# Optimization experiments

Measured on AMD Instinct MI355X. Metric: run time of the kernel, lower is better.

Reference implementation:

```python
import jax, jax.numpy as jnp
import numpy as np

B, S, D, H, E, K, F = 8, 2048, 1024, 16, 32, 8, 1024
HD = D // H
EPS = 1e-5


def _ln(x, scale, bias):
    m = jnp.mean(x, axis=-1, keepdims=True)
    v = jnp.mean(jnp.square(x - m), axis=-1, keepdims=True)
    return (x - m) * jax.lax.rsqrt(v + EPS) * scale + bias


def setup_inputs() -> dict:
    key = jax.random.key(0)
    ks = jax.random.split(key, 14)
    w = lambda k, shp: jax.random.normal(k, shp, jnp.float32) * 0.02
    return {
        "hidden_states": jax.random.normal(ks[0], (B, S, D), jnp.float32),
        "ln1_scale": jnp.ones((D,), jnp.float32),
        "ln1_bias": jnp.zeros((D,), jnp.float32),
        "wq": w(ks[1], (D, D)), "bq": jnp.zeros((D,), jnp.float32),
        "wk": w(ks[2], (D, D)), "bk": jnp.zeros((D,), jnp.float32),
        "wv": w(ks[3], (D, D)), "bv": jnp.zeros((D,), jnp.float32),
        "ln2_scale": jnp.ones((D,), jnp.float32),
        "ln2_bias": jnp.zeros((D,), jnp.float32),
        "router_w": w(ks[4], (D, E)), "router_b": jnp.zeros((E,), jnp.float32),
        "w1": w(ks[5], (E, D, F)), "b1": jnp.zeros((E, F), jnp.float32),
        "w2": w(ks[6], (E, F, D)), "b2": jnp.zeros((E, D), jnp.float32),
    }


def reference(hidden_states, ln1_scale, ln1_bias, wq, bq, wk, bk, wv, bv,
              ln2_scale, ln2_bias, router_w, router_b, w1, b1, w2, b2):
    # --- attention sub-block (faithful to source: scores are [B,S,H,H]) ---
    x = _ln(hidden_states, ln1_scale, ln1_bias)
    q = (x @ wq + bq).reshape(B, S, H, HD)
    k = (x @ wk + bk).reshape(B, S, H, HD)
    v = (x @ wv + bv).reshape(B, S, H, HD)
    scores = jnp.einsum('bshd,bsgd->bshg', q, k) / np.sqrt(HD).astype(np.float32)
    probs = jax.nn.softmax(scores, axis=-1)
    ctx = jnp.einsum('bshg,bsgd->bshd', probs, v).reshape(B, S, D)
    h1 = hidden_states + ctx
    # --- MoE sub-block: per-token top-K of E experts ---
    x2 = _ln(h1, ln2_scale, ln2_bias)
    router_probs = jax.nn.softmax(x2 @ router_w + router_b, axis=-1)  # [B,S,E]
    top_w, top_i = jax.lax.top_k(router_probs, K)
    top_w = top_w / jnp.sum(top_w, axis=-1, keepdims=True)
    # dense per-token gate over experts (zero for unselected)
    gates = jnp.sum(jax.nn.one_hot(top_i, E, dtype=x2.dtype) * top_w[..., None], axis=-2)  # [B,S,E]
    moe = jnp.zeros_like(x2)
    for e in range(E):  # fixed small expert set; unrolled under jit
        h = jax.nn.gelu(x2 @ w1[e] + b1[e], approximate=False)
        moe = moe + gates[..., e:e + 1] * (h @ w2[e] + b2[e])
    return h1 + moe
```

## Files before the change

### kernel.cpp

```cpp
#include <hip/hip_runtime.h>
#include <hip/hip_bf16.h>
#include <stdint.h>

#define TOK 16384
#define DD  1024
#define NE  32

typedef unsigned short u16;
typedef __attribute__((ext_vector_type(8))) short short8;
typedef __attribute__((ext_vector_type(4))) float f32x4;

__device__ __forceinline__ u16 f2bf(float f) {
  unsigned int u = __float_as_uint(f);
  u += 0x7fffu + ((u >> 16) & 1u);
  return (u16)(u >> 16);
}
__device__ __forceinline__ float bf2f(u16 h) {
  return __uint_as_float(((unsigned int)h) << 16);
}
__device__ __forceinline__ void gload16(const void* g, void* l) {
  __builtin_amdgcn_global_load_lds((const __attribute__((address_space(1))) void*)g,
                                   (__attribute__((address_space(3))) void*)l, 16, 0, 0);
}
__device__ __forceinline__ float fast_gelu(float v) {
  float s = v * 0.70710678118f;
  float a = fabsf(s);
  float t = 1.0f / fmaf(0.3275911f, a, 1.0f);
  float poly = t * fmaf(t, fmaf(t, fmaf(t, fmaf(t, 1.061405429f, -1.453152027f),
                                        1.421413741f), -0.284496736f), 0.254829592f);
  float er = 1.0f - poly * __expf(-s * s);
  er = copysignf(er, s);
  return 0.5f * v * (1.0f + er);
}

__global__ __launch_bounds__(256) void k_transpose(const float* __restrict__ src,
                                                   u16* __restrict__ dst, int R, int C) {
  __shared__ float tile[32][33];
  size_t mb = (size_t)blockIdx.z * R * C;
  int c0 = blockIdx.x * 32, r0 = blockIdx.y * 32;
  int tx = threadIdx.x, ty = threadIdx.y;
#pragma unroll
  for (int i = 0; i < 4; i++)
    tile[ty + i * 8][tx] = src[mb + (size_t)(r0 + ty + i * 8) * C + c0 + tx];
  __syncthreads();
#pragma unroll
  for (int i = 0; i < 4; i++) {
    float v = tile[tx][ty + i * 8];
    dst[mb + (size_t)(c0 + ty + i * 8) * R + r0 + tx] = f2bf(v);
  }
}

__global__ __launch_bounds__(256) void k_transpose_split(const float* __restrict__ src,
                                                         u16* __restrict__ hi,
                                                         u16* __restrict__ lo, int R, int C) {
  __shared__ float tile[32][33];
  int c0 = blockIdx.x * 32, r0 = blockIdx.y * 32;
  int tx = threadIdx.x, ty = threadIdx.y;
#pragma unroll
  for (int i = 0; i < 4; i++)
    tile[ty + i * 8][tx] = src[(size_t)(r0 + ty + i * 8) * C + c0 + tx];
  __syncthreads();
#pragma unroll
  for (int i = 0; i < 4; i++) {
    float v = tile[tx][ty + i * 8];
    u16 h = f2bf(v);
    u16 l = f2bf(v - bf2f(h));
    size_t idx = (size_t)(c0 + ty + i * 8) * R + r0 + tx;
    hi[idx] = h;
    lo[idx] = l;
  }
}

__global__ __launch_bounds__(256) void k_ln1(const float* __restrict__ x,
                                             const float* __restrict__ sc,
                                             const float* __restrict__ bi,
                                             u16* __restrict__ ohi, u16* __restrict__ olo) {
  __shared__ float red[10];
  int t = blockIdx.x, tid = threadIdx.x;
  size_t base = (size_t)t * DD + tid * 4;
  float4 v = *(const float4*)(x + base);
  float s1 = v.x + v.y + v.z + v.w;
  float s2 = v.x * v.x + v.y * v.y + v.z * v.z + v.w * v.w;
  for (int o = 1; o < 64; o <<= 1) { s1 += __shfl_xor(s1, o, 64); s2 += __shfl_xor(s2, o, 64); }
  int wid = tid >> 6;
  if ((tid & 63) == 0) { red[wid * 2] = s1; red[wid * 2 + 1] = s2; }
  __syncthreads();
  if (tid == 0) {
    float a = 0, b = 0;
    for (int i = 0; i < 4; i++) { a += red[i * 2]; b += red[i * 2 + 1]; }
    float mean = a * (1.f / DD);
    float var = b * (1.f / DD) - mean * mean;
    red[8] = mean; red[9] = rsqrtf(var + 1e-5f);
  }
  __syncthreads();
  float mean = red[8], rs = red[9];
  int e0 = tid * 4;
  float xv[4] = {v.x, v.y, v.z, v.w};
  ushort4 oh, ol;
  u16* ph = (u16*)&oh; u16* pl = (u16*)&ol;
#pragma unroll
  for (int i = 0; i < 4; i++) {
    float f = (xv[i] - mean) * rs * sc[e0 + i] + bi[e0 + i];
    u16 h = f2bf(f);
    ph[i] = h;
    pl[i] = f2bf(f - bf2f(h));
  }
  *(ushort4*)(ohi + base) = oh;
  *(ushort4*)(olo + base) = ol;
}

__global__ __launch_bounds__(256) void k_attn(
    const float* __restrict__ hidden, const float* __restrict__ qb,
    const float* __restrict__ kb, const float* __restrict__ vb,
    const float* __restrict__ ln2s, const float* __restrict__ ln2b,
    float* __restrict__ out, u16* __restrict__ x2hi, u16* __restrict__ x2lo) {
  __shared__ float qs[16][68], ks[16][68], vs[16][68];
  __shared__ float probs[16][17];
  __shared__ float red[12];
  int t = blockIdx.x, tid = threadIdx.x;
  size_t base = (size_t)t * DD + tid * 4;
  int hh = tid >> 4, dd = (tid & 15) * 4;
  {
    float4 q4 = *(const float4*)(qb + base);
    float4 k4 = *(const float4*)(kb + base);
    float4 v4 = *(const float4*)(vb + base);
    qs[hh][dd + 0] = q4.x; qs[hh][dd + 1] = q4.y; qs[hh][dd + 2] = q4.z; qs[hh][dd + 3] = q4.w;
    ks[hh][dd + 0] = k4.x; ks[hh][dd + 1] = k4.y; ks[hh][dd + 2] = k4.z; ks[hh][dd + 3] = k4.w;
    vs[hh][dd + 0] = v4.x; vs[hh][dd + 1] = v4.y; vs[hh][dd + 2] = v4.z; vs[hh][dd + 3] = v4.w;
  }
  __syncthreads();
  {
    int g = tid & 15;
    float s = 0.f;
#pragma unroll
    for (int d = 0; d < 64; d++) s += qs[hh][d] * ks[g][d];
    s *= 0.125f;
    float mx = s;
    for (int o = 1; o < 16; o <<= 1) mx = fmaxf(mx, __shfl_xor(mx, o, 16));
    float p = __expf(s - mx);
    float sm = p;
    for (int o = 1; o < 16; o <<= 1) sm += __shfl_xor(sm, o, 16);
    probs[hh][g] = p / sm;
  }
  __syncthreads();
  float c0 = 0, c1 = 0, c2 = 0, c3 = 0;
#pragma unroll
  for (int g = 0; g < 16; g++) {
    float pw = probs[hh][g];
    c0 += pw * vs[g][dd + 0]; c1 += pw * vs[g][dd + 1];
    c2 += pw * vs[g][dd + 2]; c3 += pw * vs[g][dd + 3];
  }
  float4 hv = *(const float4*)(hidden + base);
  float h0 = hv.x + c0, h1 = hv.y + c1, h2 = hv.z + c2, h3 = hv.w + c3;
  { float4 o4; o4.x = h0; o4.y = h1; o4.z = h2; o4.w = h3; *(float4*)(out + base) = o4; }
  float s1 = h0 + h1 + h2 + h3;
  float s2 = h0 * h0 + h1 * h1 + h2 * h2 + h3 * h3;
  for (int o = 1; o < 64; o <<= 1) { s1 += __shfl_xor(s1, o, 64); s2 += __shfl_xor(s2, o, 64); }
  int wid = tid >> 6;
  if ((tid & 63) == 0) { red[wid * 2] = s1; red[wid * 2 + 1] = s2; }
  __syncthreads();
  if (tid == 0) {
    float a = 0, b = 0;
    for (int i = 0; i < 4; i++) { a += red[i * 2]; b += red[i * 2 + 1]; }
    float mean = a * (1.f / DD);
    float var = b * (1.f / DD) - mean * mean;
    red[8] = mean; red[9] = rsqrtf(var + 1e-5f);
  }
  __syncthreads();
  float mean = red[8], rs = red[9];
  int e0 = tid * 4;
  float hvv[4] = {h0, h1, h2, h3};
  ushort4 oh, ol;
  u16* ph = (u16*)&oh; u16* pl = (u16*)&ol;
#pragma unroll
  for (int i = 0; i < 4; i++) {
    float f = (hvv[i] - mean) * rs * ln2s[e0 + i] + ln2b[e0 + i];
    u16 h = f2bf(f);
    ph[i] = h;
    pl[i] = f2bf(f - bf2f(h));
  }
  *(ushort4*)(x2hi + base) = oh;
  *(ushort4*)(x2lo + base) = ol;
}

__global__ __launch_bounds__(256) void k_router(
    const u16* __restrict__ Xhi, const u16* __restrict__ Xlo,
    const u16* __restrict__ Bh_, const u16* __restrict__ Bl_,
    const float* __restrict__ rb, float* __restrict__ logits) {
  __shared__ alignas(16) u16 Ah[64 * 32], Al[64 * 32], Bh[32 * 32], Bl[32 * 32];
  int tid = threadIdx.x;
  int w = tid >> 6, lane = tid & 63;
  int t0 = (int)blockIdx.x * 64;
  int row = tid >> 2, q = tid & 3;
  int cb = tid & 127, rowb = cb >> 2, qb2 = cb & 3;
  f32x4 acc[2];
  acc[0] = (f32x4)0.f; acc[1] = (f32x4)0.f;
  const int la = lane & 15, lk = (lane >> 4) * 8;
  const int m0 = w * 16;
  for (int kt = 0; kt < 32; kt++) {
    int k0 = kt * 32;
    __syncthreads();
    gload16(Xhi + (size_t)(t0 + row) * DD + k0 + q * 8, (char*)Ah + tid * 16);
    gload16(Xlo + (size_t)(t0 + row) * DD + k0 + q * 8, (char*)Al + tid * 16);
    if (tid < 128)
      gload16(Bh_ + (size_t)rowb * DD + k0 + qb2 * 8, (char*)Bh + cb * 16);
    else
      gload16(Bl_ + (size_t)rowb * DD + k0 + qb2 * 8, (char*)Bl + cb * 16);
    __syncthreads();
    short8 ah = *(const short8*)&Ah[(m0 + la) * 32 + lk];
    short8 al = *(const short8*)&Al[(m0 + la) * 32 + lk];
#pragma unroll
    for (int n = 0; n < 2; n++) {
      short8 bh = *(const short8*)&Bh[(n * 16 + la) * 32 + lk];
      short8 bl = *(const short8*)&Bl[(n * 16 + la) * 32 + lk];
      acc[n] = __builtin_amdgcn_mfma_f32_16x16x32_bf16(ah, bh, acc[n], 0, 0, 0);
      acc[n] = __builtin_amdgcn_mfma_f32_16x16x32_bf16(ah, bl, acc[n], 0, 0, 0);
      acc[n] = __builtin_amdgcn_mfma_f32_16x16x32_bf16(al, bh, acc[n], 0, 0, 0);
    }
  }
  int rl4 = (lane >> 4) * 4;
#pragma unroll
  for (int n = 0; n < 2; n++) {
    int col = n * 16 + la;
    float bias = rb[col];
#pragma unroll
    for (int r = 0; r < 4; r++) {
      int grow = t0 + m0 + rl4 + r;
      logits[(size_t)grow * NE + col] = acc[n][r] + bias;
    }
  }
}

__global__ void k_zero32(int* p) { int i = threadIdx.x; if (i < 32) p[i] = 0; }

__global__ __launch_bounds__(256) void k_topk(
    const float* __restrict__ logits, int* __restrict__ counts,
    int* __restrict__ lists, int* __restrict__ slots, float* __restrict__ gsel) {
  int tid = threadIdx.x;
  int t = blockIdx.x * 8 + (tid >> 5);
  int e = tid & 31;
  int sub = (tid >> 5) & 1;
  float l = logits[(size_t)t * NE + e];
  float mx = l;
  for (int o = 1; o < 32; o <<= 1) mx = fmaxf(mx, __shfl_xor(mx, o, 32));
  float p = __expf(l - mx);
  float sm = p;
  for (int o = 1; o < 32; o <<= 1) sm += __shfl_xor(sm, o, 32);
  p /= sm;
  bool sel = false;
#pragma unroll
  for (int r = 0; r < 8; r++) {
    float bv = sel ? -1.f : p;
    int bi_ = e;
    for (int o = 1; o < 32; o <<= 1) {
      float ov = __shfl_xor(bv, o, 32);
      int oi = __shfl_xor(bi_, o, 32);
      if (ov > bv || (ov == bv && oi < bi_)) { bv = ov; bi_ = oi; }
    }
    if (e == bi_) sel = true;
  }
  float ts = sel ? p : 0.f;
  for (int o = 1; o < 32; o <<= 1) ts += __shfl_xor(ts, o, 32);
  unsigned long long bm = __ballot(sel);
  unsigned m32 = (unsigned)(bm >> (sub * 32));
  if (sel) {
    int j = __popc(m32 & ((1u << e) - 1u));
    int pos = atomicAdd(&counts[e], 1);
    lists[(size_t)e * TOK + pos] = t;
    slots[t * 8 + j] = (e << 14) | pos;
    gsel[t * 8 + j] = p / ts;
  }
}

__global__ void k_scan(const int* __restrict__ counts, int* __restrict__ segoff) {
  if (threadIdx.x == 0) { int s = 0; for (int e = 0; e < NE; e++) { segoff[e] = s; s += counts[e]; } }
}

__global__ __launch_bounds__(256) void k_gemm_p(
    const u16* __restrict__ Ahi, const u16* __restrict__ Alo,
    const u16* __restrict__ qkvT,
    const float* __restrict__ bq, const float* __restrict__ bk, const float* __restrict__ bv,
    float* __restrict__ Cbase) {
  constexpr int KD = 1024;
  __shared__ alignas(16) u16 As[2][2][128 * 32];
  __shared__ alignas(16) u16 Bs[2][2][128 * 32];
  const int tid = threadIdx.x;
  const int w = tid >> 6, lane = tid & 63;
  const int bm = blockIdx.x, bn = blockIdx.y, z = blockIdx.z;
  const u16* Bhi = qkvT + (size_t)z * (2u * KD * KD);
  const u16* Blo = Bhi + (size_t)KD * KD;
  const float* bias = (z == 0) ? bq : (z == 1) ? bk : bv;
  float* C = Cbase + (size_t)z * TOK * KD;

  int rowA[2], qA[2], rowB[2];
#pragma unroll
  for (int i = 0; i < 2; i++) {
    int c = (w * 2 + i) * 64 + lane;
    int r = c >> 2;
    qA[i] = (c & 3) ^ ((c >> 3) & 3);
    rowB[i] = bn * 128 + r;
    rowA[i] = bm * 128 + r;
  }

  auto stage = [&](int buf, int k0) {
#pragma unroll
    for (int i = 0; i < 2; i++) {
      size_t ga = (size_t)rowA[i] * KD + k0 + qA[i] * 8;
      size_t gb = (size_t)rowB[i] * KD + k0 + qA[i] * 8;
      int lo_off = (w * 2 + i) * 1024;
      gload16(Ahi + ga, (char*)&As[buf][0][0] + lo_off);
      gload16(Alo + ga, (char*)&As[buf][1][0] + lo_off);
      gload16(Bhi + gb, (char*)&Bs[buf][0][0] + lo_off);
      gload16(Blo + gb, (char*)&Bs[buf][1][0] + lo_off);
    }
  };

  f32x4 acc[4][4];
#pragma unroll
  for (int m = 0; m < 4; m++)
#pragma unroll
    for (int n = 0; n < 4; n++) acc[m][n] = (f32x4)0.f;

  const int wr = (w >> 1) * 64, wc = (w & 1) * 64;
  const int la = lane & 15;
  const int sA = (((lane >> 4) ^ (((wr + la) >> 1) & 3)) * 8);
  const int sB = (((lane >> 4) ^ (((wc + la) >> 1) & 3)) * 8);

  stage(0, 0);
  __syncthreads();
  for (int kt = 0; kt < 32; kt++) {
    const int cur = kt & 1;
    if (kt + 1 < 32) stage(cur ^ 1, (kt + 1) * 32);
    short8 ah[4], al[4], bh[4], bl[4];
#pragma unroll
    for (int m = 0; m < 4; m++) {
      ah[m] = *(const short8*)&As[cur][0][(wr + m * 16 + la) * 32 + sA];
      al[m] = *(const short8*)&As[cur][1][(wr + m * 16 + la) * 32 + sA];
    }
#pragma unroll
    for (int n = 0; n < 4; n++) {
      bh[n] = *(const short8*)&Bs[cur][0][(wc + n * 16 + la) * 32 + sB];
      bl[n] = *(const short8*)&Bs[cur][1][(wc + n * 16 + la) * 32 + sB];
    }
#pragma unroll
    for (int m = 0; m < 4; m++)
#pragma unroll
      for (int n = 0; n < 4; n++) {
        acc[m][n] = __builtin_amdgcn_mfma_f32_16x16x32_bf16(ah[m], bh[n], acc[m][n], 0, 0, 0);
        acc[m][n] = __builtin_amdgcn_mfma_f32_16x16x32_bf16(ah[m], bl[n], acc[m][n], 0, 0, 0);
        acc[m][n] = __builtin_amdgcn_mfma_f32_16x16x32_bf16(al[m], bh[n], acc[m][n], 0, 0, 0);
      }
    __syncthreads();
  }

  const int rl4 = (lane >> 4) * 4;
#pragma unroll
  for (int m = 0; m < 4; m++) {
#pragma unroll
    for (int n = 0; n < 4; n++) {
      const int col = bn * 128 + wc + n * 16 + la;
      const float bvv = bias[col];
      f32x4 a4 = acc[m][n];
#pragma unroll
      for (int r = 0; r < 4; r++) {
        const int grow = bm * 128 + wr + m * 16 + rl4 + r;
        C[(size_t)grow * KD + col] = a4[r] + bvv;
      }
    }
  }
}

__global__ __launch_bounds__(256) void k_gemm1(
    const u16* __restrict__ A, const u16* __restrict__ BT, const float* __restrict__ bias,
    u16* __restrict__ Cb, const int* __restrict__ lists, const int* __restrict__ counts,
    const int* __restrict__ segoff) {
  constexpr int KD = 1024;
  __shared__ alignas(16) u16 As[2][128 * 32];
  __shared__ alignas(16) u16 Bs[2][128 * 32];

  int e = (int)blockIdx.z;
  int count = counts[e];
  if ((int)blockIdx.x * 128 >= count) return;
  const int* list = lists + (size_t)e * TOK;
  int so = segoff[e];
  const u16* Bp = BT + (size_t)e * (KD * KD);
  const float* bp = bias + (size_t)e * KD;

  const int tid = threadIdx.x;
  const int w = tid >> 6, lane = tid & 63;
  const int bm = blockIdx.x, bn = blockIdx.y;

  int rowA[2], qA[2], rowB[2];
#pragma unroll
  for (int i = 0; i < 2; i++) {
    int c = (w * 2 + i) * 64 + lane;
    int r = c >> 2;
    qA[i] = (c & 3) ^ ((c >> 3) & 3);
    rowB[i] = bn * 128 + r;
    int rr = bm * 128 + r;
    rowA[i] = (rr < count) ? list[rr] : 0;
  }

  auto stage = [&](int buf, int k0) {
#pragma unroll
    for (int i = 0; i < 2; i++) {
      gload16(A + (size_t)rowA[i] * KD + k0 + qA[i] * 8,
              (char*)&As[buf][0] + (w * 2 + i) * 1024);
      gload16(Bp + (size_t)rowB[i] * KD + k0 + qA[i] * 8,
              (char*)&Bs[buf][0] + (w * 2 + i) * 1024);
    }
  };

  f32x4 acc[4][4];
#pragma unroll
  for (int m = 0; m < 4; m++)
#pragma unroll
    for (int n = 0; n < 4; n++) acc[m][n] = (f32x4)0.f;

  const int wr = (w >> 1) * 64, wc = (w & 1) * 64;
  const int la = lane & 15;
  const int sA = (((lane >> 4) ^ (((wr + la) >> 1) & 3)) * 8);
  const int sB = (((lane >> 4) ^ (((wc + la) >> 1) & 3)) * 8);

  stage(0, 0);
  __syncthreads();
#pragma unroll 2
  for (int kt = 0; kt < 32; kt++) {
    const int cur = kt & 1;
    if (kt + 1 < 32) stage(cur ^ 1, (kt + 1) * 32);
    short8 af[4], bf8[4];
#pragma unroll
    for (int m = 0; m < 4; m++)
      af[m] = *(const short8*)&As[cur][(wr + m * 16 + la) * 32 + sA];
#pragma unroll
    for (int n = 0; n < 4; n++)
      bf8[n] = *(const short8*)&Bs[cur][(wc + n * 16 + la) * 32 + sB];
#pragma unroll
    for (int m = 0; m < 4; m++)
#pragma unroll
      for (int n = 0; n < 4; n++)
        acc[m][n] = __builtin_amdgcn_mfma_f32_16x16x32_bf16(af[m], bf8[n], acc[m][n], 0, 0, 0);
    __syncthreads();
  }

  const int rl4 = (lane >> 4) * 4;
#pragma unroll
  for (int m = 0; m < 4; m++) {
#pragma unroll
    for (int n = 0; n < 4; n++) {
      const int col = bn * 128 + wc + n * 16 + la;
      const float bvv = bp[col];
      f32x4 a4 = acc[m][n];
#pragma unroll
      for (int r = 0; r < 4; r++) {
        const int grow = bm * 128 + wr + m * 16 + rl4 + r;
        if (grow < count)
          Cb[(size_t)(so + grow) * KD + col] = f2bf(fast_gelu(a4[r] + bvv));
      }
    }
  }
}

__global__ __launch_bounds__(256) void k_gemm2(
    const u16* __restrict__ A, const u16* __restrict__ BT, const float* __restrict__ bias,
    u16* __restrict__ out2, const int* __restrict__ counts, const int* __restrict__ segoff,
    int col0, int C) {
  constexpr int KD = 1024;
  __shared__ alignas(16) u16 As[2][128 * 32];
  __shared__ alignas(16) u16 Bs[2][128 * 32];

  int e = (int)blockIdx.z;
  int count = counts[e];
  if ((int)blockIdx.x * 128 >= count) return;
  int so = segoff[e];
  const u16* Bp = BT + (size_t)e * (KD * KD);
  const float* bp = bias + (size_t)e * KD;

  const int tid = threadIdx.x;
  const int w = tid >> 6, lane = tid & 63;
  const int bm = blockIdx.x, bn = blockIdx.y;

  int rowA[2], qA[2], rowB[2];
#pragma unroll
  for (int i = 0; i < 2; i++) {
    int c = (w * 2 + i) * 64 + lane;
    int r = c >> 2;
    qA[i] = (c & 3) ^ ((c >> 3) & 3);
    rowB[i] = col0 + bn * 128 + r;
    int rr = bm * 128 + r;
    rowA[i] = so + ((rr < count) ? rr : 0);
  }

  auto stage = [&](int buf, int k0) {
#pragma unroll
    for (int i = 0; i < 2; i++) {
      gload16(A + (size_t)rowA[i] * KD + k0 + qA[i] * 8,
              (char*)&As[buf][0] + (w * 2 + i) * 1024);
      gload16(Bp + (size_t)rowB[i] * KD + k0 + qA[i] * 8,
              (char*)&Bs[buf][0] + (w * 2 + i) * 1024);
    }
  };

  f32x4 acc[4][4];
#pragma unroll
  for (int m = 0; m < 4; m++)
#pragma unroll
    for (int n = 0; n < 4; n++) acc[m][n] = (f32x4)0.f;

  const int wr = (w >> 1) * 64, wc = (w & 1) * 64;
  const int la = lane & 15;
  const int sA = (((lane >> 4) ^ (((wr + la) >> 1) & 3)) * 8);
  const int sB = (((lane >> 4) ^ (((wc + la) >> 1) & 3)) * 8);

  stage(0, 0);
  __syncthreads();
#pragma unroll 2
  for (int kt = 0; kt < 32; kt++) {
    const int cur = kt & 1;
    if (kt + 1 < 32) stage(cur ^ 1, (kt + 1) * 32);
    short8 af[4], bf8[4];
#pragma unroll
    for (int m = 0; m < 4; m++)
      af[m] = *(const short8*)&As[cur][(wr + m * 16 + la) * 32 + sA];
#pragma unroll
    for (int n = 0; n < 4; n++)
      bf8[n] = *(const short8*)&Bs[cur][(wc + n * 16 + la) * 32 + sB];
#pragma unroll
    for (int m = 0; m < 4; m++)
#pragma unroll
      for (int n = 0; n < 4; n++)
        acc[m][n] = __builtin_amdgcn_mfma_f32_16x16x32_bf16(af[m], bf8[n], acc[m][n], 0, 0, 0);
    __syncthreads();
  }

  const int rl4 = (lane >> 4) * 4;
#pragma unroll
  for (int m = 0; m < 4; m++) {
#pragma unroll
    for (int n = 0; n < 4; n++) {
      const int lcol = bn * 128 + wc + n * 16 + la;
      const float bvv = bp[col0 + lcol];
      f32x4 a4 = acc[m][n];
#pragma unroll
      for (int r = 0; r < 4; r++) {
        const int grow = bm * 128 + wr + m * 16 + rl4 + r;
        if (grow < count)
          out2[(size_t)(so + grow) * C + lcol] = f2bf(a4[r] + bvv);
      }
    }
  }
}

__global__ __launch_bounds__(256) void k_gather(
    const float* __restrict__ gsel, const int* __restrict__ slots,
    const int* __restrict__ segoff, const u16* __restrict__ out2,
    float* __restrict__ out, int col0, int C, int cshift) {
  int tid4 = threadIdx.x * 4;
  int tpb = 1024 >> cshift;
  int t = blockIdx.x * tpb + (tid4 >> cshift);
  int c4 = tid4 & (C - 1);
  float a0 = 0, a1 = 0, a2 = 0, a3 = 0;
#pragma unroll
  for (int j = 0; j < 8; j++) {
    int s = slots[t * 8 + j];
    float g = gsel[t * 8 + j];
    int seg = segoff[s >> 14] + (s & 16383);
    ushort4 v4 = *(const ushort4*)(out2 + (size_t)seg * C + c4);
    a0 += g * bf2f(v4.x); a1 += g * bf2f(v4.y);
    a2 += g * bf2f(v4.z); a3 += g * bf2f(v4.w);
  }
  size_t ob = (size_t)t * DD + col0 + c4;
  float4 o = *(const float4*)(out + ob);
  o.x += a0; o.y += a1; o.z += a2; o.w += a3;
  *(float4*)(out + ob) = o;
}

extern "C" void kernel_launch(void* const* d_in, const int* in_sizes, int n_in,
                              void* d_out, int out_size, void* d_ws, size_t ws_size,
                              hipStream_t stream) {
  (void)in_sizes; (void)n_in; (void)out_size;
  const float* hidden = (const float*)d_in[0];
  const float* ln1s = (const float*)d_in[1];
  const float* ln1b = (const float*)d_in[2];
  const float* wq = (const float*)d_in[3];
  const float* bq = (const float*)d_in[4];
  const float* wk = (const float*)d_in[5];
  const float* bk = (const float*)d_in[6];
  const float* wv = (const float*)d_in[7];
  const float* bv = (const float*)d_in[8];
  const float* ln2s = (const float*)d_in[9];
  const float* ln2b = (const float*)d_in[10];
  const float* rw = (const float*)d_in[11];
  const float* rb = (const float*)d_in[12];
  const float* w1 = (const float*)d_in[13];
  const float* b1 = (const float*)d_in[14];
  const float* w2 = (const float*)d_in[15];
  const float* b2 = (const float*)d_in[16];
  float* out = (float*)d_out;

  char* wsp = (char*)d_ws;
  size_t off = 0;
  auto alloc = [&](size_t b) -> void* {
    void* p = wsp + off;
    off += (b + 255) & ~(size_t)255;
    return p;
  };
  u16* wT = (u16*)alloc((size_t)NE * DD * DD * 2);
  int* slots = (int*)alloc((size_t)TOK * 8 * 4);
  float* gsel = (float*)alloc((size_t)TOK * 8 * 4);
  int* counts = (int*)alloc(NE * 4);
  int* segoff = (int*)alloc((NE + 1) * 4);
  u16* rwTh = (u16*)alloc((size_t)NE * DD * 2);
  u16* rwTl = (u16*)alloc((size_t)NE * DD * 2);
  float* logits = (float*)alloc((size_t)TOK * NE * 4);
  u16* x_hi = (u16*)alloc((size_t)TOK * DD * 2);
  int* lists = (int*)alloc((size_t)NE * TOK * 4);
  char* pool = (char*)alloc((size_t)TOK * 8 * DD * 2);
  u16* qkvT = (u16*)pool;
  u16* x_lo = (u16*)(pool + 12u * 1024 * 1024);
  float* qkv = (float*)(pool + 44u * 1024 * 1024);
  float* qbuf = qkv;
  float* kbuf = qkv + (size_t)TOK * DD;
  float* vbuf = qkv + 2 * (size_t)TOK * DD;
  u16* h_buf = (u16*)pool;

  const size_t ROWS = (size_t)TOK * 8;
  size_t extra = (ws_size > off) ? ws_size - off : 0;
  int C;
  u16* out2;
  if (extra >= ROWS * 1024 * 2 + 1024) { C = 1024; out2 = (u16*)alloc(ROWS * 1024 * 2); }
  else if (extra >= ROWS * 512 * 2 + 1024) { C = 512; out2 = (u16*)alloc(ROWS * 512 * 2); }
  else if (extra >= ROWS * 256 * 2 + 1024) { C = 256; out2 = (u16*)alloc(ROWS * 256 * 2); }
  else { C = 128; out2 = (u16*)x_hi; }
  int cshift = 31 - __builtin_clz((unsigned)C);

  dim3 tb32(32, 8, 1);
  k_zero32<<<1, 64, 0, stream>>>(counts);
  k_transpose_split<<<dim3(32, 32, 1), tb32, 0, stream>>>(wq, qkvT, qkvT + (size_t)DD * DD, DD, DD);
  k_transpose_split<<<dim3(32, 32, 1), tb32, 0, stream>>>(wk, qkvT + 2 * (size_t)DD * DD, qkvT + 3 * (size_t)DD * DD, DD, DD);
  k_transpose_split<<<dim3(32, 32, 1), tb32, 0, stream>>>(wv, qkvT + 4 * (size_t)DD * DD, qkvT + 5 * (size_t)DD * DD, DD, DD);
  k_transpose_split<<<dim3(1, 32, 1), tb32, 0, stream>>>(rw, rwTh, rwTl, DD, NE);
  k_transpose<<<dim3(32, 32, NE), tb32, 0, stream>>>(w1, wT, DD, DD);
  k_ln1<<<TOK, 256, 0, stream>>>(hidden, ln1s, ln1b, x_hi, x_lo);
  k_gemm_p<<<dim3(128, 8, 3), 256, 0, stream>>>(x_hi, x_lo, qkvT, bq, bk, bv, qkv);
  k_attn<<<TOK, 256, 0, stream>>>(hidden, qbuf, kbuf, vbuf, ln2s, ln2b, out, x_hi, x_lo);
  k_router<<<TOK / 64, 256, 0, stream>>>(x_hi, x_lo, rwTh, rwTl, rb, logits);
  k_topk<<<TOK / 8, 256, 0, stream>>>(logits, counts, lists, slots, gsel);
  k_scan<<<1, 32, 0, stream>>>(counts, segoff);
  k_gemm1<<<dim3(128, 8, NE), 256, 0, stream>>>(x_hi, wT, b1, h_buf, lists, counts, segoff);
  k_transpose<<<dim3(32, 32, NE), tb32, 0, stream>>>(w2, wT, DD, DD);
  for (int c0 = 0; c0 < DD; c0 += C) {
    k_gemm2<<<dim3(128, C / 128, NE), 256, 0, stream>>>(h_buf, wT, b2, out2, counts, segoff, c0, C);
    k_gather<<<TOK >> (10 - cshift), 256, 0, stream>>>(gsel, slots, segoff, out2, out, c0, C, cshift);
  }
}
```

Measured before the change: 2.061 ms.

## Merge MoE expert GEMMs into one templated 256x256-tile kernel with 8 waves

Replaces the separate gemm1/gemm2 expert kernels with a single templated kernel that uses 256x256 output tiles, 512 threads (8 waves, each computing 128x64) and a simplified XOR swizzle for LDS staging. Larger tiles raise arithmetic intensity and cut repeated global loads of the expert weights and gathered activations. The cost is twice the LDS (64KB), more accumulator registers per thread and lower occupancy, plus more wasted rows on small experts. For C=128 it launches a 256-wide tile and masks off the extra columns, reading weight rows beyond the chunk.

```diff
diff --git a/kernel.cpp b/kernel.cpp
--- a/kernel.cpp
+++ b/kernel.cpp
@@ -370,19 +370,20 @@
   }
 }
 
-__global__ __launch_bounds__(256) void k_gemm1(
+template <int MODE>
+__global__ __launch_bounds__(512) void k_moe(
     const u16* __restrict__ A, const u16* __restrict__ BT, const float* __restrict__ bias,
-    u16* __restrict__ Cb, const int* __restrict__ lists, const int* __restrict__ counts,
-    const int* __restrict__ segoff) {
+    u16* __restrict__ Cout, const int* __restrict__ lists, const int* __restrict__ counts,
+    const int* __restrict__ segoff, int col0, int C) {
   constexpr int KD = 1024;
-  __shared__ alignas(16) u16 As[2][128 * 32];
-  __shared__ alignas(16) u16 Bs[2][128 * 32];
-
-  int e = (int)blockIdx.z;
-  int count = counts[e];
-  if ((int)blockIdx.x * 128 >= count) return;
+  __shared__ alignas(16) u16 As[2][256 * 32];
+  __shared__ alignas(16) u16 Bs[2][256 * 32];
+
+  const int e = (int)blockIdx.z;
+  const int count = counts[e];
+  if ((int)blockIdx.x * 256 >= count) return;
   const int* list = lists + (size_t)e * TOK;
-  int so = segoff[e];
+  const int so = segoff[e];
   const u16* Bp = BT + (size_t)e * (KD * KD);
   const float* bp = bias + (size_t)e * KD;
 
@@ -390,162 +391,85 @@
   const int w = tid >> 6, lane = tid & 63;
   const int bm = blockIdx.x, bn = blockIdx.y;
 
-  int rowA[2], qA[2], rowB[2];
+  int rowA[2], rowB[2], qsw[2];
 #pragma unroll
   for (int i = 0; i < 2; i++) {
-    int c = (w * 2 + i) * 64 + lane;
-    int r = c >> 2;
-    qA[i] = (c & 3) ^ ((c >> 3) & 3);
-    rowB[i] = bn * 128 + r;
-    int rr = bm * 128 + r;
-    rowA[i] = (rr < count) ? list[rr] : 0;
+    int c = w * 2 + i;
+    int row = c * 16 + (lane >> 2);
+    int p = lane & 3;
+    qsw[i] = (p ^ ((row >> 1) & 3)) * 8;
+    int rr = bm * 256 + row;
+    int rrc = (rr < count) ? rr : (count - 1);
+    if constexpr (MODE == 1) {
+      rowA[i] = list[rrc];
+      rowB[i] = bn * 256 + row;
+    } else {
+      rowA[i] = so + rrc;
+      rowB[i] = col0 + bn * 256 + row;
+    }
   }
 
   auto stage = [&](int buf, int k0) {
 #pragma unroll
     for (int i = 0; i < 2; i++) {
-      gload16(A + (size_t)rowA[i] * KD + k0 + qA[i] * 8,
-              (char*)&As[buf][0] + (w * 2 + i) * 1024);
-      gload16(Bp + (size_t)rowB[i] * KD + k0 + qA[i] * 8,
-              (char*)&Bs[buf][0] + (w * 2 + i) * 1024);
+      int c = w * 2 + i;
+      gload16(A + (size_t)rowA[i] * KD + k0 + qsw[i], (char*)&As[buf][0] + c * 1024);
+      gload16(Bp + (size_t)rowB[i] * KD + k0 + qsw[i], (char*)&Bs[buf][0] + c * 1024);
     }
   };
 
-  f32x4 acc[4][4];
-#pragma unroll
-  for (int m = 0; m < 4; m++)
+  f32x4 acc[8][4];
+#pragma unroll
+  for (int m = 0; m < 8; m++)
 #pragma unroll
     for (int n = 0; n < 4; n++) acc[m][n] = (f32x4)0.f;
 
-  const int wr = (w >> 1) * 64, wc = (w & 1) * 64;
-  const int la = lane & 15;
-  const int sA = (((lane >> 4) ^ (((wr + la) >> 1) & 3)) * 8);
-  const int sB = (((lane >> 4) ^ (((wc + la) >> 1) & 3)) * 8);
+  const int wr = w >> 2, wc = w & 3;
+  const int la = lane & 15, hi = lane >> 4;
+  const int sxor = hi ^ ((la >> 1) & 3);
 
   stage(0, 0);
   __syncthreads();
-#pragma unroll 2
   for (int kt = 0; kt < 32; kt++) {
     const int cur = kt & 1;
     if (kt + 1 < 32) stage(cur ^ 1, (kt + 1) * 32);
-    short8 af[4], bf8[4];
-#pragma unroll
-    for (int m = 0; m < 4; m++)
-      af[m] = *(const short8*)&As[cur][(wr + m * 16 + la) * 32 + sA];
-#pragma unroll
-    for (int n = 0; n < 4; n++)
-      bf8[n] = *(const short8*)&Bs[cur][(wc + n * 16 + la) * 32 + sB];
-#pragma unroll
-    for (int m = 0; m < 4; m++)
+    short8 bfr[4];
+#pragma unroll
+    for (int n = 0; n < 4; n++) {
+      int rowb = wc * 64 + n * 16 + la;
+      bfr[n] = *(const short8*)&Bs[cur][rowb * 32 + sxor * 8];
+    }
+#pragma unroll
+    for (int m = 0; m < 8; m++) {
+      int rowa = wr * 128 + m * 16 + la;
+      short8 af = *(const short8*)&As[cur][rowa * 32 + sxor * 8];
 #pragma unroll
       for (int n = 0; n < 4; n++)
-        acc[m][n] = __builtin_amdgcn_mfma_f32_16x16x32_bf16(af[m], bf8[n], acc[m][n], 0, 0, 0);
+        acc[m][n] = __builtin_amdgcn_mfma_f32_16x16x32_bf16(af, bfr[n], acc[m][n], 0, 0, 0);
+    }
     __syncthreads();
   }
 
-  const int rl4 = (lane >> 4) * 4;
-#pragma unroll
-  for (int m = 0; m < 4; m++) {
+#pragma unroll
+  for (int m = 0; m < 8; m++) {
 #pragma unroll
     for (int n = 0; n < 4; n++) {
-      const int col = bn * 128 + wc + n * 16 + la;
-      const float bvv = bp[col];
+      const int lcol = bn * 256 + wc * 64 + n * 16 + la;
       f32x4 a4 = acc[m][n];
 #pragma unroll
       for (int r = 0; r < 4; r++) {
-        const int grow = bm * 128 + wr + m * 16 + rl4 + r;
-        if (grow < count)
-          Cb[(size_t)(so + grow) * KD + col] = f2bf(fast_gelu(a4[r] + bvv));
-      }
-    }
-  }
-}
-
-__global__ __launch_bounds__(256) void k_gemm2(
-    const u16* __restrict__ A, const u16* __restrict__ BT, const float* __restrict__ bias,
-    u16* __restrict__ out2, const int* __restrict__ counts, const int* __restrict__ segoff,
-    int col0, int C) {
-  constexpr int KD = 1024;
-  __shared__ alignas(16) u16 As[2][128 * 32];
-  __shared__ alignas(16) u16 Bs[2][128 * 32];
-
-  int e = (int)blockIdx.z;
-  int count = counts[e];
-  if ((int)blockIdx.x * 128 >= count) return;
-  int so = segoff[e];
-  const u16* Bp = BT + (size_t)e * (KD * KD);
-  const float* bp = bias + (size_t)e * KD;
-
-  const int tid = threadIdx.x;
-  const int w = tid >> 6, lane = tid & 63;
-  const int bm = blockIdx.x, bn = blockIdx.y;
-
-  int rowA[2], qA[2], rowB[2];
-#pragma unroll
-  for (int i = 0; i < 2; i++) {
-    int c = (w * 2 + i) * 64 + lane;
-    int r = c >> 2;
-    qA[i] = (c & 3) ^ ((c >> 3) & 3);
-    rowB[i] = col0 + bn * 128 + r;
-    int rr = bm * 128 + r;
-    rowA[i] = so + ((rr < count) ? rr : 0);
-  }
-
-  auto stage = [&](int buf, int k0) {
-#pragma unroll
-    for (int i = 0; i < 2; i++) {
-      gload16(A + (size_t)rowA[i] * KD + k0 + qA[i] * 8,
-              (char*)&As[buf][0] + (w * 2 + i) * 1024);
-      gload16(Bp + (size_t)rowB[i] * KD + k0 + qA[i] * 8,
-              (char*)&Bs[buf][0] + (w * 2 + i) * 1024);
-    }
-  };
-
-  f32x4 acc[4][4];
-#pragma unroll
-  for (int m = 0; m < 4; m++)
-#pragma unroll
-    for (int n = 0; n < 4; n++) acc[m][n] = (f32x4)0.f;
-
-  const int wr = (w >> 1) * 64, wc = (w & 1) * 64;
-  const int la = lane & 15;
-  const int sA = (((lane >> 4) ^ (((wr + la) >> 1) & 3)) * 8);
-  const int sB = (((lane >> 4) ^ (((wc + la) >> 1) & 3)) * 8);
-
-  stage(0, 0);
-  __syncthreads();
-#pragma unroll 2
-  for (int kt = 0; kt < 32; kt++) {
-    const int cur = kt & 1;
-    if (kt + 1 < 32) stage(cur ^ 1, (kt + 1) * 32);
-    short8 af[4], bf8[4];
-#pragma unroll
-    for (int m = 0; m < 4; m++)
-      af[m] = *(const short8*)&As[cur][(wr + m * 16 + la) * 32 + sA];
-#pragma unroll
-    for (int n = 0; n < 4; n++)
-      bf8[n] = *(const short8*)&Bs[cur][(wc + n * 16 + la) * 32 + sB];
-#pragma unroll
-    for (int m = 0; m < 4; m++)
-#pragma unroll
-      for (int n = 0; n < 4; n++)
-        acc[m][n] = __builtin_amdgcn_mfma_f32_16x16x32_bf16(af[m], bf8[n], acc[m][n], 0, 0, 0);
-    __syncthreads();
-  }
-
-  const int rl4 = (lane >> 4) * 4;
-#pragma unroll
-  for (int m = 0; m < 4; m++) {
-#pragma unroll
-    for (int n = 0; n < 4; n++) {
-      const int lcol = bn * 128 + wc + n * 16 + la;
-      const float bvv = bp[col0 + lcol];
-      f32x4 a4 = acc[m][n];
-#pragma unroll
-      for (int r = 0; r < 4; r++) {
-        const int grow = bm * 128 + wr + m * 16 + rl4 + r;
-        if (grow < count)
-          out2[(size_t)(so + grow) * C + lcol] = f2bf(a4[r] + bvv);
+        const int grow = bm * 256 + wr * 128 + m * 16 + hi * 4 + r;
+        if (grow < count) {
+          if constexpr (MODE == 1) {
+            float v = a4[r] + bp[lcol];
+            Cout[(size_t)(so + grow) * KD + lcol] = f2bf(fast_gelu(v));
+          } else {
+            if (lcol < C) {
+              float v = a4[r] + bp[col0 + lcol];
+              Cout[(size_t)(so + grow) * C + lcol] = f2bf(v);
+            }
+          }
+        }
       }
     }
   }
@@ -647,10 +571,11 @@
   k_router<<<TOK / 64, 256, 0, stream>>>(x_hi, x_lo, rwTh, rwTl, rb, logits);
   k_topk<<<TOK / 8, 256, 0, stream>>>(logits, counts, lists, slots, gsel);
   k_scan<<<1, 32, 0, stream>>>(counts, segoff);
-  k_gemm1<<<dim3(128, 8, NE), 256, 0, stream>>>(x_hi, wT, b1, h_buf, lists, counts, segoff);
+  k_moe<1><<<dim3(64, 4, NE), 512, 0, stream>>>(x_hi, wT, b1, h_buf, lists, counts, segoff, 0, DD);
   k_transpose<<<dim3(32, 32, NE), tb32, 0, stream>>>(w2, wT, DD, DD);
   for (int c0 = 0; c0 < DD; c0 += C) {
-    k_gemm2<<<dim3(128, C / 128, NE), 256, 0, stream>>>(h_buf, wT, b2, out2, counts, segoff, c0, C);
+    int bnv = (C >= 256) ? (C / 256) : 1;
+    k_moe<2><<<dim3(64, bnv, NE), 512, 0, stream>>>(h_buf, wT, b2, out2, lists, counts, segoff, c0, C);
     k_gather<<<TOK >> (10 - cshift), 256, 0, stream>>>(gsel, slots, segoff, out2, out, c0, C, cshift);
   }
 }
```

Result: slower. 2.976 ms (+44.4%).

## Rewrite attention kernel as one wavefront per token using cross-lane shuffles

Applied to the files above, without the earlier changes.

The per-token attention/LN2 kernel moves from one 256-thread block per token, which staged q/k/v in shared memory and needed several __syncthreads, to one 64-lane wavefront per token with four tokens per block. Head-to-head scores and the probability-weighted V sum are computed from registers using __shfl, and the LN2 reduction becomes wave-local. This removes LDS traffic, block barriers and the shared reduction. In exchange it adds many shuffle instructions and higher register use per lane, and the kernel is a small part of the total runtime.

```diff
diff --git a/kernel.cpp b/kernel.cpp
--- a/kernel.cpp
+++ b/kernel.cpp
@@ -8,6 +8,7 @@
 
 typedef unsigned short u16;
 typedef __attribute__((ext_vector_type(8))) short short8;
+typedef __attribute__((ext_vector_type(8))) unsigned short u16x8;
 typedef __attribute__((ext_vector_type(4))) float f32x4;
 
 __device__ __forceinline__ u16 f2bf(float f) {
@@ -114,73 +115,106 @@
     const float* __restrict__ kb, const float* __restrict__ vb,
     const float* __restrict__ ln2s, const float* __restrict__ ln2b,
     float* __restrict__ out, u16* __restrict__ x2hi, u16* __restrict__ x2lo) {
-  __shared__ float qs[16][68], ks[16][68], vs[16][68];
-  __shared__ float probs[16][17];
-  __shared__ float red[12];
-  int t = blockIdx.x, tid = threadIdx.x;
-  size_t base = (size_t)t * DD + tid * 4;
-  int hh = tid >> 4, dd = (tid & 15) * 4;
-  {
-    float4 q4 = *(const float4*)(qb + base);
-    float4 k4 = *(const float4*)(kb + base);
-    float4 v4 = *(const float4*)(vb + base);
-    qs[hh][dd + 0] = q4.x; qs[hh][dd + 1] = q4.y; qs[hh][dd + 2] = q4.z; qs[hh][dd + 3] = q4.w;
-    ks[hh][dd + 0] = k4.x; ks[hh][dd + 1] = k4.y; ks[hh][dd + 2] = k4.z; ks[hh][dd + 3] = k4.w;
-    vs[hh][dd + 0] = v4.x; vs[hh][dd + 1] = v4.y; vs[hh][dd + 2] = v4.z; vs[hh][dd + 3] = v4.w;
-  }
-  __syncthreads();
-  {
-    int g = tid & 15;
-    float s = 0.f;
-#pragma unroll
-    for (int d = 0; d < 64; d++) s += qs[hh][d] * ks[g][d];
-    s *= 0.125f;
-    float mx = s;
-    for (int o = 1; o < 16; o <<= 1) mx = fmaxf(mx, __shfl_xor(mx, o, 16));
-    float p = __expf(s - mx);
-    float sm = p;
-    for (int o = 1; o < 16; o <<= 1) sm += __shfl_xor(sm, o, 16);
-    probs[hh][g] = p / sm;
-  }
-  __syncthreads();
-  float c0 = 0, c1 = 0, c2 = 0, c3 = 0;
+  int tid = threadIdx.x;
+  int w = tid >> 6, lane = tid & 63;
+  int t = blockIdx.x * 4 + w;
+  int j = lane & 3;
+  size_t base = (size_t)t * DD + lane * 16;
+
+  float4 qf[4], kf[4], vf[4], hf[4];
+#pragma unroll
+  for (int i = 0; i < 4; i++) {
+    qf[i] = *(const float4*)(qb + base + i * 4);
+    kf[i] = *(const float4*)(kb + base + i * 4);
+    vf[i] = *(const float4*)(vb + base + i * 4);
+    hf[i] = *(const float4*)(hidden + base + i * 4);
+  }
+
+  float s[16];
 #pragma unroll
   for (int g = 0; g < 16; g++) {
-    float pw = probs[hh][g];
-    c0 += pw * vs[g][dd + 0]; c1 += pw * vs[g][dd + 1];
-    c2 += pw * vs[g][dd + 2]; c3 += pw * vs[g][dd + 3];
-  }
-  float4 hv = *(const float4*)(hidden + base);
-  float h0 = hv.x + c0, h1 = hv.y + c1, h2 = hv.z + c2, h3 = hv.w + c3;
-  { float4 o4; o4.x = h0; o4.y = h1; o4.z = h2; o4.w = h3; *(float4*)(out + base) = o4; }
-  float s1 = h0 + h1 + h2 + h3;
-  float s2 = h0 * h0 + h1 * h1 + h2 * h2 + h3 * h3;
+    int src = g * 4 + j;
+    float acc = 0.f;
+#pragma unroll
+    for (int i = 0; i < 4; i++) {
+      float4 kg;
+      kg.x = __shfl(kf[i].x, src, 64);
+      kg.y = __shfl(kf[i].y, src, 64);
+      kg.z = __shfl(kf[i].z, src, 64);
+      kg.w = __shfl(kf[i].w, src, 64);
+      acc += qf[i].x * kg.x + qf[i].y * kg.y + qf[i].z * kg.z + qf[i].w * kg.w;
+    }
+    s[g] = acc;
+  }
+#pragma unroll
+  for (int g = 0; g < 16; g++) {
+    s[g] += __shfl_xor(s[g], 1, 64);
+    s[g] += __shfl_xor(s[g], 2, 64);
+    s[g] *= 0.125f;
+  }
+  float mx = s[0];
+#pragma unroll
+  for (int g = 1; g < 16; g++) mx = fmaxf(mx, s[g]);
+  float sum = 0.f;
+#pragma unroll
+  for (int g = 0; g < 16; g++) { s[g] = __expf(s[g] - mx); sum += s[g]; }
+  float inv = 1.0f / sum;
+
+  float c16[16];
+#pragma unroll
+  for (int i = 0; i < 16; i++) c16[i] = 0.f;
+#pragma unroll
+  for (int g = 0; g < 16; g++) {
+    int src = g * 4 + j;
+    float p = s[g] * inv;
+#pragma unroll
+    for (int i = 0; i < 4; i++) {
+      float4 vg;
+      vg.x = __shfl(vf[i].x, src, 64);
+      vg.y = __shfl(vf[i].y, src, 64);
+      vg.z = __shfl(vf[i].z, src, 64);
+      vg.w = __shfl(vf[i].w, src, 64);
+      c16[i * 4 + 0] += p * vg.x;
+      c16[i * 4 + 1] += p * vg.y;
+      c16[i * 4 + 2] += p * vg.z;
+      c16[i * 4 + 3] += p * vg.w;
+    }
+  }
+  float h1[16];
+#pragma unroll
+  for (int i = 0; i < 4; i++) {
+    float4 o4;
+    o4.x = hf[i].x + c16[i * 4 + 0];
+    o4.y = hf[i].y + c16[i * 4 + 1];
+    o4.z = hf[i].z + c16[i * 4 + 2];
+    o4.w = hf[i].w + c16[i * 4 + 3];
+    h1[i * 4 + 0] = o4.x; h1[i * 4 + 1] = o4.y; h1[i * 4 + 2] = o4.z; h1[i * 4 + 3] = o4.w;
+    *(float4*)(out + base + i * 4) = o4;
+  }
+  float s1 = 0.f, s2 = 0.f;
+#pragma unroll
+  for (int i = 0; i < 16; i++) { s1 += h1[i]; s2 += h1[i] * h1[i]; }
   for (int o = 1; o < 64; o <<= 1) { s1 += __shfl_xor(s1, o, 64); s2 += __shfl_xor(s2, o, 64); }
-  int wid = tid >> 6;
-  if ((tid & 63) == 0) { red[wid * 2] = s1; red[wid * 2 + 1] = s2; }
-  __syncthreads();
-  if (tid == 0) {
-    float a = 0, b = 0;
-    for (int i = 0; i < 4; i++) { a += red[i * 2]; b += red[i * 2 + 1]; }
-    float mean = a * (1.f / DD);
-    float var = b * (1.f / DD) - mean * mean;
-    red[8] = mean; red[9] = rsqrtf(var + 1e-5f);
-  }
-  __syncthreads();
-  float mean = red[8], rs = red[9];
-  int e0 = tid * 4;
-  float hvv[4] = {h0, h1, h2, h3};
-  ushort4 oh, ol;
-  u16* ph = (u16*)&oh; u16* pl = (u16*)&ol;
-#pragma unroll
-  for (int i = 0; i < 4; i++) {
-    float f = (hvv[i] - mean) * rs * ln2s[e0 + i] + ln2b[e0 + i];
+  float mean = s1 * (1.f / DD);
+  float var = s2 * (1.f / DD) - mean * mean;
+  float rs = rsqrtf(var + 1e-5f);
+
+  u16 oh2[16], ol2[16];
+#pragma unroll
+  for (int i = 0; i < 16; i++) {
+    float f = (h1[i] - mean) * rs * ln2s[lane * 16 + i] + ln2b[lane * 16 + i];
     u16 h = f2bf(f);
-    ph[i] = h;
-    pl[i] = f2bf(f - bf2f(h));
-  }
-  *(ushort4*)(x2hi + base) = oh;
-  *(ushort4*)(x2lo + base) = ol;
+    oh2[i] = h;
+    ol2[i] = f2bf(f - bf2f(h));
+  }
+#pragma unroll
+  for (int half = 0; half < 2; half++) {
+    u16x8 oh, ol;
+#pragma unroll
+    for (int i = 0; i < 8; i++) { oh[i] = oh2[half * 8 + i]; ol[i] = ol2[half * 8 + i]; }
+    *(u16x8*)(x2hi + base + half * 8) = oh;
+    *(u16x8*)(x2lo + base + half * 8) = ol;
+  }
 }
 
 __global__ __launch_bounds__(256) void k_router(
@@ -643,7 +677,7 @@
   k_transpose<<<dim3(32, 32, NE), tb32, 0, stream>>>(w1, wT, DD, DD);
   k_ln1<<<TOK, 256, 0, stream>>>(hidden, ln1s, ln1b, x_hi, x_lo);
   k_gemm_p<<<dim3(128, 8, 3), 256, 0, stream>>>(x_hi, x_lo, qkvT, bq, bk, bv, qkv);
-  k_attn<<<TOK, 256, 0, stream>>>(hidden, qbuf, kbuf, vbuf, ln2s, ln2b, out, x_hi, x_lo);
+  k_attn<<<TOK / 4, 256, 0, stream>>>(hidden, qbuf, kbuf, vbuf, ln2s, ln2b, out, x_hi, x_lo);
   k_router<<<TOK / 64, 256, 0, stream>>>(x_hi, x_lo, rwTh, rwTl, rb, logits);
   k_topk<<<TOK / 8, 256, 0, stream>>>(logits, counts, lists, slots, gsel);
   k_scan<<<1, 32, 0, stream>>>(counts, segoff);
```

After: 2.096 ms. No clear change (+1.7%).
